# Kernel tuning notes

Hardware: AMD Instinct MI355X
Metric: run time of the kernel (lower is better)

The kernel has to match this reference:

```python
import jax, jax.numpy as jnp
import numpy as np

DIM = 1024
HEADS = 16
HEAD_DIM = DIM // HEADS
SCALE = HEAD_DIM ** -0.5


def setup_inputs() -> dict:
    key = jax.random.key(0)
    k1, k2, k3 = jax.random.split(key, 3)
    x = jax.random.normal(k1, (4, 2048, DIM), dtype=jnp.float32)
    Wqkv = jax.random.normal(k2, (DIM, 3 * DIM), dtype=jnp.float32) * (DIM ** -0.5)
    Wout = jax.random.normal(k3, (DIM, DIM), dtype=jnp.float32) * (DIM ** -0.5)
    bout = jnp.zeros((DIM,), dtype=jnp.float32)
    return {"x": x, "Wqkv": Wqkv, "Wout": Wout, "bout": bout}


def reference(x, Wqkv, Wout, bout):
    b, n, _ = x.shape
    qkv = x @ Wqkv  # [b, n, 3*dim]
    q, k, v = jnp.split(qkv, 3, axis=-1)
    # [b, n, dim] -> [b, h, n, d]
    def split_heads(t):
        return t.reshape(b, n, HEADS, HEAD_DIM).transpose(0, 2, 1, 3)
    q, k, v = split_heads(q), split_heads(k), split_heads(v)
    dots = jnp.einsum('bhid,bhjd->bhij', q, k) * SCALE
    attn = jax.nn.softmax(dots, axis=-1)
    out = jnp.einsum('bhij,bhjd->bhid', attn, v)
    out = out.transpose(0, 2, 1, 3).reshape(b, n, DIM)
    return out @ Wout + bout  # dropout is identity in eval mode
```

## Files before the change

kernel.cpp:

```cpp
#include <hip/hip_runtime.h>
#include <hip/hip_bf16.h>

#define BATCH 4
#define SEQ   2048
#define DIM   1024
#define HEADS 16
#define HD    64
#define ROWS  (BATCH * SEQ)
#define QKV_N (3 * DIM)
#define ATT_C 0.18033688011f

typedef unsigned short u16;
typedef _Float16 half8 __attribute__((ext_vector_type(8)));
typedef _Float16 half4v __attribute__((ext_vector_type(4)));
typedef float f32x4 __attribute__((ext_vector_type(4)));

__device__ __forceinline__ void gload_lds16(const u16* g, u16* l) {
  typedef const __attribute__((address_space(1))) unsigned int* gp_t;
  typedef __attribute__((address_space(3))) unsigned int* lp_t;
  __builtin_amdgcn_global_load_lds((gp_t)(const void*)g, (lp_t)(void*)l, 16, 0, 0);
}

__global__ __launch_bounds__(256) void conv_x(const float* __restrict__ x,
                                              u16* __restrict__ xh) {
  int i = blockIdx.x * 256 + threadIdx.x;
  float4 v = ((const float4*)x)[i];
  half4v h = {(_Float16)v.x, (_Float16)v.y, (_Float16)v.z, (_Float16)v.w};
  *(half4v*)&xh[(size_t)i * 4] = h;
}

__global__ __launch_bounds__(256) void conv_w(const float* __restrict__ W,
                                              u16* __restrict__ Wt,
                                              int K, int N) {
  __shared__ float T[64][65];
  const int tid = threadIdx.x;
  const int k0 = blockIdx.y * 64, n0 = blockIdx.x * 64;
#pragma unroll
  for (int j = 0; j < 4; ++j) {
    int k = j * 16 + (tid >> 4), n4 = (tid & 15) * 4;
    float4 v = *(const float4*)(W + (size_t)(k0 + k) * N + n0 + n4);
    T[k][n4 + 0] = v.x; T[k][n4 + 1] = v.y; T[k][n4 + 2] = v.z; T[k][n4 + 3] = v.w;
  }
  __syncthreads();
#pragma unroll
  for (int j = 0; j < 4; ++j) {
    int n = j * 16 + (tid >> 4), k4 = (tid & 15) * 4;
    half4v w = {(_Float16)T[k4 + 0][n], (_Float16)T[k4 + 1][n],
                (_Float16)T[k4 + 2][n], (_Float16)T[k4 + 3][n]};
    *(half4v*)&Wt[(size_t)(n0 + n) * K + k0 + k4] = w;
  }
}

template <int MODE>
__global__ __launch_bounds__(256) void gemm_bt(
    const u16* __restrict__ A, const u16* __restrict__ Bt,
    const float* __restrict__ bias, void* __restrict__ Cv,
    u16* __restrict__ Qg, u16* __restrict__ Kg, u16* __restrict__ VtG,
    int M, int N, int K) {
  __shared__ u16 As[128 * 32];
  __shared__ u16 Bs[128 * 32];

  const int tid = threadIdx.x;
  const int wave = tid >> 6, lane = tid & 63;
  const int q4 = lane >> 4, c = lane & 15;
  const int wm = wave >> 1, wn = wave & 1;
  const int row0 = blockIdx.y * 128, col0 = blockIdx.x * 128;
  const int rr = lane >> 2, seg = lane & 3;

  f32x4 acc[4][4];
#pragma unroll
  for (int mi = 0; mi < 4; ++mi)
#pragma unroll
    for (int ni = 0; ni < 4; ++ni) acc[mi][ni] = (f32x4){0.f, 0.f, 0.f, 0.f};

  for (int k0 = 0; k0 < K; k0 += 32) {
#pragma unroll
    for (int i = 0; i < 2; ++i) {
      int chunk = wave * 2 + i;
      gload_lds16(A + (size_t)(row0 + chunk * 16 + rr) * K + k0 + seg * 8,
                  &As[chunk * 512]);
      gload_lds16(Bt + (size_t)(col0 + chunk * 16 + rr) * K + k0 + seg * 8,
                  &Bs[chunk * 512]);
    }
    __syncthreads();

    half8 af[4], bf[4];
#pragma unroll
    for (int mi = 0; mi < 4; ++mi)
      af[mi] = *(const half8*)&As[(wm * 64 + mi * 16 + c) * 32 + q4 * 8];
#pragma unroll
    for (int ni = 0; ni < 4; ++ni)
      bf[ni] = *(const half8*)&Bs[(wn * 64 + ni * 16 + c) * 32 + q4 * 8];
#pragma unroll
    for (int mi = 0; mi < 4; ++mi)
#pragma unroll
      for (int ni = 0; ni < 4; ++ni)
        acc[mi][ni] = __builtin_amdgcn_mfma_f32_16x16x32_f16(
            af[mi], bf[ni], acc[mi][ni], 0, 0, 0);
    __syncthreads();
  }

#pragma unroll
  for (int mi = 0; mi < 4; ++mi)
#pragma unroll
    for (int ni = 0; ni < 4; ++ni) {
      int colg = col0 + wn * 64 + ni * 16 + c;
      if (MODE == 0) {
        float bv = bias[colg];
#pragma unroll
        for (int r = 0; r < 4; ++r) {
          int rowg = row0 + wm * 64 + mi * 16 + q4 * 4 + r;
          ((float*)Cv)[(size_t)rowg * N + colg] = acc[mi][ni][r] + bv;
        }
      } else {
        int rowg0 = row0 + wm * 64 + mi * 16 + q4 * 4;
        int b  = rowg0 >> 11;
        int which = colg >> 10;
        int rem = colg & 1023;
        int hh = rem >> 6, d = rem & 63;
        size_t bh = (size_t)(b * HEADS + hh);
        if (which == 2) {
          int i0 = rowg0 & 2047;
          half4v pv = {(_Float16)acc[mi][ni][0], (_Float16)acc[mi][ni][1],
                       (_Float16)acc[mi][ni][2], (_Float16)acc[mi][ni][3]};
          *(half4v*)&VtG[(bh * HD + d) * SEQ + i0] = pv;
        } else {
          u16* dst = (which == 0) ? Qg : Kg;
          float sc = (which == 0) ? ATT_C : 1.0f;
#pragma unroll
          for (int r = 0; r < 4; ++r) {
            int i = (rowg0 + r) & 2047;
            ((_Float16*)dst)[(bh * SEQ + i) * HD + d] =
                (_Float16)(acc[mi][ni][r] * sc);
          }
        }
      }
    }
}

#define PSTR 140

__global__ __launch_bounds__(512, 4) void attn_mfma(
    const u16* __restrict__ Qg, const u16* __restrict__ Kg,
    const u16* __restrict__ VtG, u16* __restrict__ ctx) {
  const int L  = blockIdx.x;
  const int bh = L & 63;
  const int b  = bh >> 4, h = bh & 15;
  const int qt = L >> 6;

  __shared__ u16 Ks[2][128 * 32];
  __shared__ u16 Vt[4][64 * 32];
  __shared__ u16 Ps[128 * PSTR];
  __shared__ float lred[8][128];
  __shared__ float lfull[128];

  const int tid  = threadIdx.x;
  const int wave = tid >> 6;
  const int lane = tid & 63;
  const int q4   = lane >> 4;
  const int c    = lane & 15;
  const int rr   = lane >> 2, seg = lane & 3;
  const int sseg = seg ^ (rr & 3);
  const int rsw  = (c & 3);

  const size_t bhb = (size_t)bh;
  const int qrow0 = qt * 128;

  half8 qf[8][2];
#pragma unroll
  for (int nt = 0; nt < 8; ++nt)
#pragma unroll
    for (int kh = 0; kh < 2; ++kh)
      qf[nt][kh] = *(const half8*)&Qg[(bhb * SEQ + qrow0 + nt * 16 + c) * HD
                                      + kh * 32 + q4 * 8];

  f32x4 o_acc[4];
#pragma unroll
  for (int dt = 0; dt < 4; ++dt) o_acc[dt] = (f32x4){0.f, 0.f, 0.f, 0.f};
  float lp[8] = {0.f, 0.f, 0.f, 0.f, 0.f, 0.f, 0.f, 0.f};

  for (int j0 = 0; j0 < SEQ; j0 += 128) {
    __syncthreads();

#pragma unroll
    for (int i = 0; i < 2; ++i) {
      int chunk = wave * 2 + i;
      int kh = chunk >> 3, jr = chunk & 7;
      gload_lds16(Kg + (bhb * SEQ + j0 + jr * 16 + rr) * HD + kh * 32 + sseg * 8,
                  &Ks[kh][jr * 16 * 32]);
      int q = chunk >> 2, d16 = chunk & 3;
      gload_lds16(VtG + (bhb * HD + d16 * 16 + rr) * SEQ + j0 + q * 32 + sseg * 8,
                  &Vt[q][d16 * 16 * 32]);
    }
    __syncthreads();

    half8 af0 = *(const half8*)&Ks[0][(wave * 16 + c) * 32 + (q4 ^ rsw) * 8];
    half8 af1 = *(const half8*)&Ks[1][(wave * 16 + c) * 32 + (q4 ^ rsw) * 8];
#pragma unroll
    for (int nt = 0; nt < 8; ++nt) {
      f32x4 st = (f32x4){0.f, 0.f, 0.f, 0.f};
      st = __builtin_amdgcn_mfma_f32_16x16x32_f16(af0, qf[nt][0], st, 0, 0, 0);
      st = __builtin_amdgcn_mfma_f32_16x16x32_f16(af1, qf[nt][1], st, 0, 0, 0);
      float p0 = __builtin_amdgcn_exp2f(st[0]);
      float p1 = __builtin_amdgcn_exp2f(st[1]);
      float p2 = __builtin_amdgcn_exp2f(st[2]);
      float p3 = __builtin_amdgcn_exp2f(st[3]);
      lp[nt] += (p0 + p1) + (p2 + p3);
      half4v w = {(_Float16)p0, (_Float16)p1, (_Float16)p2, (_Float16)p3};
      *(half4v*)&Ps[(nt * 16 + c) * PSTR + wave * 16 + q4 * 4] = w;
    }
    __syncthreads();

#pragma unroll
    for (int kc = 0; kc < 4; ++kc) {
      half8 pa = *(const half8*)&Ps[(wave * 16 + c) * PSTR + kc * 32 + q4 * 8];
#pragma unroll
      for (int dt = 0; dt < 4; ++dt) {
        half8 vb = *(const half8*)&Vt[kc][(dt * 16 + c) * 32 + (q4 ^ rsw) * 8];
        o_acc[dt] = __builtin_amdgcn_mfma_f32_16x16x32_f16(
            pa, vb, o_acc[dt], 0, 0, 0);
      }
    }
  }

#pragma unroll
  for (int nt = 0; nt < 8; ++nt) {
    lp[nt] += __shfl_xor(lp[nt], 16);
    lp[nt] += __shfl_xor(lp[nt], 32);
  }
  if (q4 == 0)
#pragma unroll
    for (int nt = 0; nt < 8; ++nt) lred[wave][nt * 16 + c] = lp[nt];
  __syncthreads();
  if (tid < 128) {
    float s = 0.f;
#pragma unroll
    for (int w = 0; w < 8; ++w) s += lred[w][tid];
    lfull[tid] = s;
  }
  __syncthreads();

#pragma unroll
  for (int r = 0; r < 4; ++r) {
    int i = wave * 16 + q4 * 4 + r;
    float inv = 1.0f / lfull[i];
    size_t row = (size_t)b * SEQ + qrow0 + i;
#pragma unroll
    for (int dt = 0; dt < 4; ++dt)
      ((_Float16*)ctx)[row * DIM + h * HD + dt * 16 + c] =
          (_Float16)(o_acc[dt][r] * inv);
  }
}

extern "C" void kernel_launch(void* const* d_in, const int* in_sizes, int n_in,
                              void* d_out, int out_size, void* d_ws, size_t ws_size,
                              hipStream_t stream) {
  const float* x    = (const float*)d_in[0];
  const float* Wqkv = (const float*)d_in[1];
  const float* Wout = (const float*)d_in[2];
  const float* bout = (const float*)d_in[3];
  float* out = (float*)d_out;

  u16* xh   = (u16*)d_ws;
  u16* Wqt  = xh  + (size_t)ROWS * DIM;
  u16* Wot  = Wqt + (size_t)QKV_N * DIM;
  u16* Qg   = Wot + (size_t)DIM * DIM;
  u16* Kg   = Qg  + (size_t)BATCH * HEADS * SEQ * HD;
  u16* VtG  = Kg  + (size_t)BATCH * HEADS * SEQ * HD;
  u16* ctxh = VtG + (size_t)BATCH * HEADS * HD * SEQ;

  conv_x<<<ROWS * DIM / 4 / 256, 256, 0, stream>>>(x, xh);
  conv_w<<<dim3(QKV_N / 64, DIM / 64), 256, 0, stream>>>(Wqkv, Wqt, DIM, QKV_N);
  conv_w<<<dim3(DIM / 64, DIM / 64), 256, 0, stream>>>(Wout, Wot, DIM, DIM);

  gemm_bt<1><<<dim3(QKV_N / 128, ROWS / 128), 256, 0, stream>>>(
      xh, Wqt, nullptr, nullptr, Qg, Kg, VtG, ROWS, QKV_N, DIM);

  attn_mfma<<<dim3(1024), 512, 0, stream>>>(Qg, Kg, VtG, ctxh);

  gemm_bt<0><<<dim3(DIM / 128, ROWS / 128), 256, 0, stream>>>(
      ctxh, Wot, bout, out, nullptr, nullptr, nullptr, ROWS, DIM, DIM);
}
```

Baseline: 304.4 us.

## Keep attention probabilities in registers via lane permutes instead of LDS

Restructures the attention kernel so each wave owns 16 query rows and computes S^T tiles over key chunks, then rearranges the exponentiated probabilities between lanes with permlane32_swap and shuffles to form the MFMA operand directly. This removes the shared-memory P buffer, one barrier per key tile, and the cross-wave row-sum reduction through LDS. Less LDS use allows raising occupancy to 6 blocks per CU, and the K/V swizzle pattern is changed to match. The cost is extra permute and shuffle instructions per tile and more complex lane bookkeeping.

```diff
diff --git a/kernel.cpp b/kernel.cpp
--- a/kernel.cpp
+++ b/kernel.cpp
@@ -14,6 +14,7 @@
 typedef _Float16 half8 __attribute__((ext_vector_type(8)));
 typedef _Float16 half4v __attribute__((ext_vector_type(4)));
 typedef float f32x4 __attribute__((ext_vector_type(4)));
+typedef unsigned int uint2v __attribute__((ext_vector_type(2)));
 
 __device__ __forceinline__ void gload_lds16(const u16* g, u16* l) {
   typedef const __attribute__((address_space(1))) unsigned int* gp_t;
@@ -138,9 +139,7 @@
     }
 }
 
-#define PSTR 140
-
-__global__ __launch_bounds__(512, 4) void attn_mfma(
+__global__ __launch_bounds__(512, 6) void attn_mfma(
     const u16* __restrict__ Qg, const u16* __restrict__ Kg,
     const u16* __restrict__ VtG, u16* __restrict__ ctx) {
   const int L  = blockIdx.x;
@@ -150,9 +149,6 @@
 
   __shared__ u16 Ks[2][128 * 32];
   __shared__ u16 Vt[4][64 * 32];
-  __shared__ u16 Ps[128 * PSTR];
-  __shared__ float lred[8][128];
-  __shared__ float lfull[128];
 
   const int tid  = threadIdx.x;
   const int wave = tid >> 6;
@@ -160,24 +156,19 @@
   const int q4   = lane >> 4;
   const int c    = lane & 15;
   const int rr   = lane >> 2, seg = lane & 3;
-  const int sseg = seg ^ (rr & 3);
-  const int rsw  = (c & 3);
+  const int sseg = seg ^ ((rr >> 1) & 3);
+  const int xsw  = (q4 ^ ((c >> 1) & 3)) * 8;
 
   const size_t bhb = (size_t)bh;
-  const int qrow0 = qt * 128;
-
-  half8 qf[8][2];
-#pragma unroll
-  for (int nt = 0; nt < 8; ++nt)
-#pragma unroll
-    for (int kh = 0; kh < 2; ++kh)
-      qf[nt][kh] = *(const half8*)&Qg[(bhb * SEQ + qrow0 + nt * 16 + c) * HD
-                                      + kh * 32 + q4 * 8];
+  const int qrow0 = qt * 128 + wave * 16;
+
+  half8 qf0 = *(const half8*)&Qg[(bhb * SEQ + qrow0 + c) * HD + q4 * 8];
+  half8 qf1 = *(const half8*)&Qg[(bhb * SEQ + qrow0 + c) * HD + 32 + q4 * 8];
 
   f32x4 o_acc[4];
 #pragma unroll
   for (int dt = 0; dt < 4; ++dt) o_acc[dt] = (f32x4){0.f, 0.f, 0.f, 0.f};
-  float lp[8] = {0.f, 0.f, 0.f, 0.f, 0.f, 0.f, 0.f, 0.f};
+  float lp = 0.f;
 
   for (int j0 = 0; j0 < SEQ; j0 += 128) {
     __syncthreads();
@@ -194,61 +185,68 @@
     }
     __syncthreads();
 
-    half8 af0 = *(const half8*)&Ks[0][(wave * 16 + c) * 32 + (q4 ^ rsw) * 8];
-    half8 af1 = *(const half8*)&Ks[1][(wave * 16 + c) * 32 + (q4 ^ rsw) * 8];
-#pragma unroll
-    for (int nt = 0; nt < 8; ++nt) {
-      f32x4 st = (f32x4){0.f, 0.f, 0.f, 0.f};
-      st = __builtin_amdgcn_mfma_f32_16x16x32_f16(af0, qf[nt][0], st, 0, 0, 0);
-      st = __builtin_amdgcn_mfma_f32_16x16x32_f16(af1, qf[nt][1], st, 0, 0, 0);
-      float p0 = __builtin_amdgcn_exp2f(st[0]);
-      float p1 = __builtin_amdgcn_exp2f(st[1]);
-      float p2 = __builtin_amdgcn_exp2f(st[2]);
-      float p3 = __builtin_amdgcn_exp2f(st[3]);
-      lp[nt] += (p0 + p1) + (p2 + p3);
-      half4v w = {(_Float16)p0, (_Float16)p1, (_Float16)p2, (_Float16)p3};
-      *(half4v*)&Ps[(nt * 16 + c) * PSTR + wave * 16 + q4 * 4] = w;
-    }
-    __syncthreads();
-
 #pragma unroll
     for (int kc = 0; kc < 4; ++kc) {
-      half8 pa = *(const half8*)&Ps[(wave * 16 + c) * PSTR + kc * 32 + q4 * 8];
+      const int ro0 = (kc * 32 + c) * 32 + xsw;
+      const int ro1 = (kc * 32 + 16 + c) * 32 + xsw;
+      half8 a00 = *(const half8*)&Ks[0][ro0];
+      half8 a01 = *(const half8*)&Ks[1][ro0];
+      half8 a10 = *(const half8*)&Ks[0][ro1];
+      half8 a11 = *(const half8*)&Ks[1][ro1];
+      f32x4 st0 = (f32x4){0.f, 0.f, 0.f, 0.f};
+      f32x4 st1 = (f32x4){0.f, 0.f, 0.f, 0.f};
+      st0 = __builtin_amdgcn_mfma_f32_16x16x32_f16(a00, qf0, st0, 0, 0, 0);
+      st0 = __builtin_amdgcn_mfma_f32_16x16x32_f16(a01, qf1, st0, 0, 0, 0);
+      st1 = __builtin_amdgcn_mfma_f32_16x16x32_f16(a10, qf0, st1, 0, 0, 0);
+      st1 = __builtin_amdgcn_mfma_f32_16x16x32_f16(a11, qf1, st1, 0, 0, 0);
+
+      float p0 = __builtin_amdgcn_exp2f(st0[0]);
+      float p1 = __builtin_amdgcn_exp2f(st0[1]);
+      float p2 = __builtin_amdgcn_exp2f(st0[2]);
+      float p3 = __builtin_amdgcn_exp2f(st0[3]);
+      float p4 = __builtin_amdgcn_exp2f(st1[0]);
+      float p5 = __builtin_amdgcn_exp2f(st1[1]);
+      float p6 = __builtin_amdgcn_exp2f(st1[2]);
+      float p7 = __builtin_amdgcn_exp2f(st1[3]);
+      lp += ((p0 + p1) + (p2 + p3)) + ((p4 + p5) + (p6 + p7));
+
+      union { half4v h; unsigned int w[2]; } ea, eb;
+      ea.h = (half4v){(_Float16)p0, (_Float16)p1, (_Float16)p2, (_Float16)p3};
+      eb.h = (half4v){(_Float16)p4, (_Float16)p5, (_Float16)p6, (_Float16)p7};
+      uint2v s0 = __builtin_amdgcn_permlane32_swap(ea.w[0], eb.w[0], false, false);
+      uint2v s1 = __builtin_amdgcn_permlane32_swap(ea.w[1], eb.w[1], false, false);
+      unsigned int A0 = s0[0], B0 = s0[1];
+      unsigned int A1 = s1[0], B1 = s1[1];
+      unsigned int Xs0 = __shfl_xor(A0, 16);
+      unsigned int Xs1 = __shfl_xor(A1, 16);
+      unsigned int Ys0 = __shfl_xor(B0, 16);
+      unsigned int Ys1 = __shfl_xor(B1, 16);
+      union { half8 h; unsigned int w[4]; } pb;
+      const bool odd = (q4 & 1);
+      pb.w[0] = odd ? Ys0 : A0;
+      pb.w[1] = odd ? Ys1 : A1;
+      pb.w[2] = odd ? B0  : Xs0;
+      pb.w[3] = odd ? B1  : Xs1;
+
 #pragma unroll
       for (int dt = 0; dt < 4; ++dt) {
-        half8 vb = *(const half8*)&Vt[kc][(dt * 16 + c) * 32 + (q4 ^ rsw) * 8];
+        half8 vb = *(const half8*)&Vt[kc][(dt * 16 + c) * 32 + xsw];
         o_acc[dt] = __builtin_amdgcn_mfma_f32_16x16x32_f16(
-            pa, vb, o_acc[dt], 0, 0, 0);
+            vb, pb.h, o_acc[dt], 0, 0, 0);
       }
     }
   }
 
-#pragma unroll
-  for (int nt = 0; nt < 8; ++nt) {
-    lp[nt] += __shfl_xor(lp[nt], 16);
-    lp[nt] += __shfl_xor(lp[nt], 32);
-  }
-  if (q4 == 0)
-#pragma unroll
-    for (int nt = 0; nt < 8; ++nt) lred[wave][nt * 16 + c] = lp[nt];
-  __syncthreads();
-  if (tid < 128) {
-    float s = 0.f;
-#pragma unroll
-    for (int w = 0; w < 8; ++w) s += lred[w][tid];
-    lfull[tid] = s;
-  }
-  __syncthreads();
-
-#pragma unroll
-  for (int r = 0; r < 4; ++r) {
-    int i = wave * 16 + q4 * 4 + r;
-    float inv = 1.0f / lfull[i];
-    size_t row = (size_t)b * SEQ + qrow0 + i;
-#pragma unroll
-    for (int dt = 0; dt < 4; ++dt)
-      ((_Float16*)ctx)[row * DIM + h * HD + dt * 16 + c] =
-          (_Float16)(o_acc[dt][r] * inv);
+  lp += __shfl_xor(lp, 16);
+  lp += __shfl_xor(lp, 32);
+  float inv = 1.0f / lp;
+
+  size_t row = (size_t)b * SEQ + qrow0 + c;
+#pragma unroll
+  for (int dt = 0; dt < 4; ++dt) {
+    half4v o = {(_Float16)(o_acc[dt][0] * inv), (_Float16)(o_acc[dt][1] * inv),
+                (_Float16)(o_acc[dt][2] * inv), (_Float16)(o_acc[dt][3] * inv)};
+    *(half4v*)&((_Float16*)ctx)[row * DIM + h * HD + dt * 16 + q4 * 4] = o;
   }
 }
 
```

Result: no change. 303.1 us (-0.4%).
